# Performance work log

Measured on AMD Instinct MI355X. Metric: run time of the kernel, lower is better.

Reference implementation:

```python
import jax, jax.numpy as jnp
import numpy as np

N = 30000      # input points
M = 7500       # sampled queries = floor(N * ratio), ratio=0.25
K = 16         # neighbors per query
D_X = 64       # input feature dim
D_REL = 64     # point_pos_nn output dim
D_F = D_X + D_REL  # fij_hat dim = 128


def setup_inputs() -> dict:
    key = jax.random.key(0)
    ks = jax.random.split(key, 6)
    x = jax.random.normal(ks[0], (N, D_X), jnp.float32)
    pos = jax.random.normal(ks[1], (N, 3), jnp.float32)
    idx = jax.random.randint(ks[2], (M,), 0, N)
    W_pos = jax.random.normal(ks[3], (10, D_REL), jnp.float32) / jnp.sqrt(10.0)
    b_pos = jnp.zeros((D_REL,), jnp.float32)
    W_att = jax.random.normal(ks[4], (D_F, D_F), jnp.float32) / jnp.sqrt(float(D_F))
    b_att = jnp.zeros((D_F,), jnp.float32)
    W_glob = jax.random.normal(ks[5], (D_F, D_F), jnp.float32) / jnp.sqrt(float(D_F))
    b_glob = jnp.zeros((D_F,), jnp.float32)
    return {"x": x, "pos": pos, "idx": idx, "W_pos": W_pos, "b_pos": b_pos,
            "W_att": W_att, "b_att": b_att, "W_glob": W_glob, "b_glob": b_glob}


def reference(x, pos, idx, W_pos, b_pos, W_att, b_att, W_glob, b_glob):
    # --- KNN: brute-force squared distances from sampled queries to all points ---
    pos_q = pos[idx]                                         # [M, 3]
    d2 = ((pos_q * pos_q).sum(-1)[:, None]
          + (pos * pos).sum(-1)[None, :]
          - 2.0 * pos_q @ pos.T)                             # [M, N]
    _, nbr = jax.lax.top_k(-d2, K)                           # [M, K] neighbor indices

    # --- Local Spatial Encoding (message) ---
    pos_j = pos[nbr]                                         # [M, K, 3]
    pos_i = jnp.broadcast_to(pos_q[:, None, :], pos_j.shape) # [M, K, 3]
    vij = pos_i - pos_j                                      # [M, K, 3]
    dij = jnp.linalg.norm(vij, axis=-1, keepdims=True)       # [M, K, 1]
    rel = jnp.concatenate([pos_i, pos_j, vij, dij], axis=-1) # [M, K, 10]
    rij = jax.nn.relu(rel @ W_pos + b_pos)                   # [M, K, D_REL]

    # --- Attentive pooling ---
    fij = jnp.concatenate([x[nbr], rij], axis=-1)            # [M, K, D_F]
    g = fij @ W_att + b_att                                  # [M, K, D_F]
    s = jax.nn.softmax(g, axis=-1)                           # softmax over feature dim
    aggr = jnp.mean(s * fij, axis=1)                         # mean over K neighbors -> [M, D_F]

    # --- global_nn (update) ---
    return jax.nn.relu(aggr @ W_glob + b_glob)               # [M, D_F]
```

## Files before the change

kernel.cpp:

```cpp
#include <hip/hip_runtime.h>
#include <stdint.h>

#define KNB     16
#define GD      64
#define GTOT    (GD * GD * GD)
#define GORIG   (-6.5f)
#define GEDGE   0.203125f
#define GINV    (1.0f / GEDGE)
#define CAPW    640
#define PROBE_T 48

typedef short short8 __attribute__((ext_vector_type(8)));
typedef float floatx4 __attribute__((ext_vector_type(4)));

__device__ __forceinline__ unsigned short f2bf(float x) {
  union { float f; uint32_t u; } v; v.f = x;
  uint32_t u = v.u + 0x7FFFu + ((v.u >> 16) & 1u);
  return (unsigned short)(u >> 16);
}
__device__ __forceinline__ float bf2f(unsigned short b) {
  return __uint_as_float(((uint32_t)b) << 16);
}
__device__ __forceinline__ int cellco(float v) {
  int c = (int)floorf((v - GORIG) * GINV);
  return c < 0 ? 0 : (c > GD - 1 ? GD - 1 : c);
}

__global__ void zero_kernel(int* __restrict__ count) {
  int i = (blockIdx.x * 256 + threadIdx.x) * 4;
  *(int4*)(count + i) = make_int4(0, 0, 0, 0);
}

__global__ void prep_kernel(const float* __restrict__ x,
                            const float* __restrict__ pos,
                            const float* __restrict__ W_att,
                            unsigned short* __restrict__ xb,
                            float4* __restrict__ pos4,
                            unsigned short* __restrict__ Wt,
                            int* __restrict__ ptcell,
                            int* __restrict__ count, int N) {
  int id = blockIdx.x * 256 + threadIdx.x;
  int nx8 = N * 8;
  if (id < nx8) {
    const float4* src = (const float4*)x + (size_t)id * 2;
    float4 a = src[0], b = src[1];
    short8 v;
    v[0] = (short)f2bf(a.x); v[1] = (short)f2bf(a.y);
    v[2] = (short)f2bf(a.z); v[3] = (short)f2bf(a.w);
    v[4] = (short)f2bf(b.x); v[5] = (short)f2bf(b.y);
    v[6] = (short)f2bf(b.z); v[7] = (short)f2bf(b.w);
    *(short8*)(xb + (size_t)id * 8) = v;
  } else if (id < nx8 + N) {
    int j = id - nx8;
    float px = pos[3 * j], py = pos[3 * j + 1], pz = pos[3 * j + 2];
    float pp = fmaf(px, px, fmaf(py, py, pz * pz));
    pos4[j] = make_float4(px, py, pz, pp);
    int cid = (cellco(pz) * GD + cellco(py)) * GD + cellco(px);
    ptcell[j] = cid;
    atomicAdd(&count[cid], 1);
  } else if (id < nx8 + N + 128 * 128) {
    int t = id - nx8 - N;
    int c = t >> 7, f = t & 127;
    Wt[f * 128 + c] = f2bf(W_att[t]);
  }
}

__global__ __launch_bounds__(256) void scan1(const int* __restrict__ count,
                                             int* __restrict__ partial) {
  int b = blockIdx.x, t = threadIdx.x;
  int v = count[b * 256 + t];
#pragma unroll
  for (int off = 1; off < 64; off <<= 1) v += __shfl_xor(v, off);
  __shared__ int ws_[4];
  if ((t & 63) == 0) ws_[t >> 6] = v;
  __syncthreads();
  if (t == 0) partial[b] = ws_[0] + ws_[1] + ws_[2] + ws_[3];
}

__global__ __launch_bounds__(256) void scan2(int* __restrict__ partial,
                                             int* __restrict__ cell_start) {
  int t = threadIdx.x;
  int v0 = partial[t * 4], v1 = partial[t * 4 + 1];
  int v2 = partial[t * 4 + 2], v3 = partial[t * 4 + 3];
  int s1 = v0 + v1, s2 = s1 + v2, s3 = s2 + v3;
  int x = s3;
  int lane = t & 63, wv = t >> 6;
#pragma unroll
  for (int off = 1; off < 64; off <<= 1) {
    int y = __shfl_up(x, off);
    if (lane >= off) x += y;
  }
  __shared__ int wsum[4];
  if (lane == 63) wsum[wv] = x;
  __syncthreads();
  int base = 0;
  for (int k = 0; k < wv; ++k) base += wsum[k];
  int excl = base + x - s3;
  partial[t * 4]     = excl;
  partial[t * 4 + 1] = excl + v0;
  partial[t * 4 + 2] = excl + s1;
  partial[t * 4 + 3] = excl + s2;
  if (t == 255) cell_start[GTOT] = excl + s3;
}

__global__ __launch_bounds__(256) void scan3(const int* __restrict__ count,
                                             const int* __restrict__ partial,
                                             int* __restrict__ cell_start,
                                             int* __restrict__ cursor) {
  int b = blockIdx.x, t = threadIdx.x;
  int v = count[b * 256 + t];
  int x = v;
  int lane = t & 63, wv = t >> 6;
#pragma unroll
  for (int off = 1; off < 64; off <<= 1) {
    int y = __shfl_up(x, off);
    if (lane >= off) x += y;
  }
  __shared__ int wsum[4];
  if (lane == 63) wsum[wv] = x;
  __syncthreads();
  int base = partial[b];
  for (int k = 0; k < wv; ++k) base += wsum[k];
  int excl = base + x - v;
  cell_start[b * 256 + t] = excl;
  cursor[b * 256 + t] = excl;
}

__global__ void scatter_kernel(const float4* __restrict__ pos4,
                               const int* __restrict__ ptcell,
                               int* __restrict__ cursor,
                               float4* __restrict__ spos4,
                               int* __restrict__ sid, int N) {
  int j = blockIdx.x * 256 + threadIdx.x;
  if (j >= N) return;
  int cid = ptcell[j];
  int slot = atomicAdd(&cursor[cid], 1);
  spos4[slot] = pos4[j];
  sid[slot] = j;
}

__global__ __launch_bounds__(256) void vscan_x(const int* __restrict__ count,
                                               int* __restrict__ V) {
  int row = blockIdx.x * 4 + (threadIdx.x >> 6);
  int ln = threadIdx.x & 63;
  int i = row * GD + ln;
  int v = count[i];
#pragma unroll
  for (int off = 1; off < 64; off <<= 1) {
    int y = __shfl_up(v, off);
    if (ln >= off) v += y;
  }
  V[i] = v;
}

__global__ __launch_bounds__(256) void vscan_y(int* __restrict__ V) {
  int pair = blockIdx.x * 4 + (threadIdx.x >> 6);
  int z = pair >> 6, x = pair & 63;
  int ln = threadIdx.x & 63;
  int i = (z * GD + ln) * GD + x;
  int v = V[i];
#pragma unroll
  for (int off = 1; off < 64; off <<= 1) {
    int y = __shfl_up(v, off);
    if (ln >= off) v += y;
  }
  V[i] = v;
}

__global__ __launch_bounds__(256) void vscan_z(int* __restrict__ V) {
  int pair = blockIdx.x * 4 + (threadIdx.x >> 6);
  int ln = threadIdx.x & 63;
  int i = ln * GD * GD + pair;
  int v = V[i];
#pragma unroll
  for (int off = 1; off < 64; off <<= 1) {
    int y = __shfl_up(v, off);
    if (ln >= off) v += y;
  }
  V[i] = v;
}

__device__ __forceinline__ unsigned long long top16_reg(
    unsigned long long* candw, int tot, int ln) {
  unsigned long long c[CAPW / 64];
#pragma unroll
  for (int chk = 0; chk < CAPW / 64; ++chk) {
    int slot = chk * 64 + ln;
    c[chk] = (slot < tot) ? candw[slot] : ~0ull;
  }
  unsigned long long mykey = ~0ull, last = 0;
#pragma unroll
  for (int r = 0; r < KNB; ++r) {
    unsigned long long mn = c[0];
#pragma unroll
    for (int chk = 1; chk < CAPW / 64; ++chk) mn = (c[chk] < mn) ? c[chk] : mn;
#pragma unroll
    for (int off = 1; off < 64; off <<= 1) {
      unsigned long long o = __shfl_xor(mn, off);
      mn = (o < mn) ? o : mn;
    }
    if (ln == r) mykey = mn;
    last = mn;
#pragma unroll
    for (int chk = 0; chk < CAPW / 64; ++chk)
      if (c[chk] == mn) c[chk] = ~0ull;
  }
  if (ln < KNB) candw[ln] = mykey;
  return last;
}

__device__ __forceinline__ void drain_annulus(
    const float4* __restrict__ spos4, const int* __restrict__ sid,
    const int* __restrict__ cell_start, unsigned long long* candw,
    uint32_t* rsAw, uint32_t* rlAw, uint32_t* rsBw, uint32_t* rpsw,
    float4 qp, int cqx, int cqy, int cqz, int slo, int shi, int ln,
    int& tot, unsigned long long& taukey) {
  const int z0 = (cqz - shi < 0) ? 0 : cqz - shi;
  const int z1 = (cqz + shi > GD - 1) ? GD - 1 : cqz + shi;
  const int y0 = (cqy - shi < 0) ? 0 : cqy - shi;
  const int y1 = (cqy + shi > GD - 1) ? GD - 1 : cqy + shi;
  const int wy = y1 - y0 + 1;
  const int npair = (z1 - z0 + 1) * wy;
  for (int base = 0; base < npair; base += 64) {
    int i = base + ln;
    int stA = 0, lA = 0, stB = 0, lB = 0;
    if (i < npair) {
      int zz = z0 + i / wy;
      int yy = y0 + (i - (i / wy) * wy);
      int dz = zz - cqz, dy = yy - cqy;
      int az = dz < 0 ? -dz : dz, ay = dy < 0 ? -dy : dy;
      int ch = az > ay ? az : ay;
      int rowbase = (zz * GD + yy) * GD;
      if (ch > slo) {
        int x0 = cqx - shi; if (x0 < 0) x0 = 0;
        int x1 = cqx + shi; if (x1 > GD - 1) x1 = GD - 1;
        stA = cell_start[rowbase + x0];
        lA  = cell_start[rowbase + x1 + 1] - stA;
      } else {
        int xl0 = cqx - shi; if (xl0 < 0) xl0 = 0;
        int xl1 = cqx - slo - 1;
        if (xl1 >= xl0) {
          stA = cell_start[rowbase + xl0];
          lA  = cell_start[rowbase + xl1 + 1] - stA;
        }
        int xr0 = cqx + slo + 1;
        int xr1 = cqx + shi; if (xr1 > GD - 1) xr1 = GD - 1;
        if (xr1 >= xr0) {
          stB = cell_start[rowbase + xr0];
          lB  = cell_start[rowbase + xr1 + 1] - stB;
        }
      }
    }
    int len = lA + lB;
    int xinc = len;
#pragma unroll
    for (int off = 1; off < 64; off <<= 1) {
      int y = __shfl_up(xinc, off);
      if (ln >= off) xinc += y;
    }
    int T = __shfl(xinc, 63);
    if (T == 0) continue;
    rpsw[ln] = (uint32_t)(xinc - len);
    rsAw[ln] = (uint32_t)stA;
    rlAw[ln] = (uint32_t)lA;
    rsBw[ln] = (uint32_t)stB;
    for (int b2 = 0; b2 < T; b2 += 64) {
      if (tot + 64 > CAPW) {
        taukey = top16_reg(candw, tot, ln);
        tot = KNB;
      }
      int flat = b2 + ln;
      unsigned long long key = ~0ull;
      bool ok = false;
      if (flat < T) {
        int lo = 0;
#pragma unroll
        for (int step = 32; step > 0; step >>= 1) {
          int mid = lo + step;
          if (mid <= 63 && (int)rpsw[mid] <= flat) lo = mid;
        }
        int o = flat - (int)rpsw[lo];
        uint32_t sa = rsAw[lo], la = rlAw[lo];
        int p = (o < (int)la) ? (int)(sa + o)
                              : (int)(rsBw[lo] + (uint32_t)(o - (int)la));
        float4 pj = spos4[p];
        float dot = fmaf(qp.x, pj.x, fmaf(qp.y, pj.y, qp.z * pj.z));
        float tt  = fmaf(-2.f, dot, pj.w);
        float d2  = fmaxf(qp.w + tt, 0.f);
        key = ((unsigned long long)__float_as_uint(d2) << 32) |
              (uint32_t)sid[p];
        ok = key < taukey;
      }
      unsigned long long bm = __ballot(ok);
      int pos = __popcll(bm & ((1ull << ln) - 1ull));
      if (ok) candw[tot + pos] = key;
      tot += __popcll(bm);
    }
  }
}

__global__ __launch_bounds__(256) void knn_grid(
    const float4* __restrict__ pos4, const float4* __restrict__ spos4,
    const int* __restrict__ sid, const int* __restrict__ cell_start,
    const int* __restrict__ V, const int* __restrict__ idx,
    int* __restrict__ nbr, int M) {
  __shared__ unsigned long long cand[4][CAPW];
  __shared__ uint32_t rsA[4][64], rlA[4][64], rsB[4][64], rps[4][64];
  const int tid = threadIdx.x, wv = tid >> 6, ln = tid & 63;
  const int m = blockIdx.x * 4 + wv;
  if (m >= M) return;

  const float4 qp = pos4[idx[m]];
  const int cqx = cellco(qp.x), cqy = cellco(qp.y), cqz = cellco(qp.z);

  int s0;
  {
    int s = ln;
    int xh = cqx + s > GD - 1 ? GD - 1 : cqx + s;
    int yh = cqy + s > GD - 1 ? GD - 1 : cqy + s;
    int zh = cqz + s > GD - 1 ? GD - 1 : cqz + s;
    int xm = cqx - s - 1, ym = cqy - s - 1, zm = cqz - s - 1;
    int c = V[(zh * GD + yh) * GD + xh];
    if (zm >= 0) c -= V[(zm * GD + yh) * GD + xh];
    if (ym >= 0) c -= V[(zh * GD + ym) * GD + xh];
    if (xm >= 0) c -= V[(zh * GD + yh) * GD + xm];
    if (zm >= 0 && ym >= 0) c += V[(zm * GD + ym) * GD + xh];
    if (zm >= 0 && xm >= 0) c += V[(zm * GD + yh) * GD + xm];
    if (ym >= 0 && xm >= 0) c += V[(zh * GD + ym) * GD + xm];
    if (zm >= 0 && ym >= 0 && xm >= 0) c -= V[(zm * GD + ym) * GD + xm];
    unsigned long long bm = __ballot(c >= PROBE_T);
    s0 = __ffsll((unsigned long long)bm) - 1;
  }

  int tot = 0;
  unsigned long long taukey = ~0ull;
  drain_annulus(spos4, sid, cell_start, &cand[wv][0], &rsA[wv][0],
                &rlA[wv][0], &rsB[wv][0], &rps[wv][0], qp, cqx, cqy, cqz,
                -1, s0, ln, tot, taukey);
  taukey = top16_reg(&cand[wv][0], tot, ln);
  tot = KNB;
  float d16sq = __uint_as_float((uint32_t)(taukey >> 32));

  int s1 = s0;
  {
    float fx = qp.x - GORIG, fy = qp.y - GORIG, fz = qp.z - GORIG;
    while (s1 < GD - 1) {
      float r = 3.0e38f;
      if (cqx - s1 > 0)      r = fminf(r, fx - (float)(cqx - s1) * GEDGE);
      if (cqx + s1 < GD - 1) r = fminf(r, (float)(cqx + s1 + 1) * GEDGE - fx);
      if (cqy - s1 > 0)      r = fminf(r, fy - (float)(cqy - s1) * GEDGE);
      if (cqy + s1 < GD - 1) r = fminf(r, (float)(cqy + s1 + 1) * GEDGE - fy);
      if (cqz - s1 > 0)      r = fminf(r, fz - (float)(cqz - s1) * GEDGE);
      if (cqz + s1 < GD - 1) r = fminf(r, (float)(cqz + s1 + 1) * GEDGE - fz);
      float r2 = (r > 1.0e19f) ? 3.0e38f : r * r;
      if (r2 >= d16sq) break;
      ++s1;
    }
  }

  if (s1 > s0) {
    drain_annulus(spos4, sid, cell_start, &cand[wv][0], &rsA[wv][0],
                  &rlA[wv][0], &rsB[wv][0], &rps[wv][0], qp, cqx, cqy, cqz,
                  s0, s1, ln, tot, taukey);
    if (tot > KNB) (void)top16_reg(&cand[wv][0], tot, ln);
  }

  if (ln < KNB) nbr[m * KNB + ln] = (int)(uint32_t)cand[wv][ln];
}

__global__ __launch_bounds__(256) void mid_kernel(
    const unsigned short* __restrict__ xb, const float4* __restrict__ pos4,
    const int* __restrict__ idx, const float* __restrict__ W_pos,
    const float* __restrict__ b_pos, const unsigned short* __restrict__ Wt,
    const float* __restrict__ b_att, const int* __restrict__ nbr,
    float* __restrict__ aggr, int M) {
  __shared__ __align__(16) unsigned short fijb[8][16][136];
  __shared__ int nbr_s[128];
  __shared__ float4 qpos_s[8];

  const int tid = threadIdx.x;
  const int wid = tid >> 6, lane = tid & 63;
  const int col = lane & 15, quad = lane >> 4;
  const int b = blockIdx.x;

  if (tid < 128) {
    int mq = b * 8 + (tid >> 4); if (mq >= M) mq = M - 1;
    nbr_s[tid] = nbr[mq * 16 + (tid & 15)];
  }
  if (tid < 8) {
    int mq = b * 8 + tid; if (mq >= M) mq = M - 1;
    qpos_s[tid] = pos4[idx[mq]];
  }
  float wp[10];
#pragma unroll
  for (int t = 0; t < 10; ++t) wp[t] = W_pos[t * 64 + lane];
  float bp = b_pos[lane];
  __syncthreads();

  {
    int rr = tid >> 1, h = tid & 1;
    int jn = nbr_s[rr];
    const short8* src = (const short8*)(xb + ((size_t)jn << 6) + (h << 5));
    short8 v0 = src[0], v1 = src[1], v2 = src[2], v3 = src[3];
    short8* dst = (short8*)&fijb[rr >> 4][rr & 15][h * 32];
    dst[0] = v0; dst[1] = v1; dst[2] = v2; dst[3] = v3;
  }
#pragma unroll
  for (int qi = 0; qi < 2; ++qi) {
    int q = wid * 2 + qi;
    float4 qp = qpos_s[q];
#pragma unroll 4
    for (int k = 0; k < 16; ++k) {
      int jn = nbr_s[q * 16 + k];
      float4 pj = pos4[jn];
      float vx = qp.x - pj.x, vy = qp.y - pj.y, vz = qp.z - pj.z;
      float dd = sqrtf(fmaf(vx, vx, fmaf(vy, vy, vz * vz)));
      float r = bp;
      r = fmaf(qp.x, wp[0], r); r = fmaf(qp.y, wp[1], r); r = fmaf(qp.z, wp[2], r);
      r = fmaf(pj.x, wp[3], r); r = fmaf(pj.y, wp[4], r); r = fmaf(pj.z, wp[5], r);
      r = fmaf(vx, wp[6], r);  r = fmaf(vy, wp[7], r);  r = fmaf(vz, wp[8], r);
      r = fmaf(dd, wp[9], r);
      r = fmaxf(r, 0.f);
      fijb[q][k][64 + lane] = f2bf(r);
    }
  }
  __syncthreads();

#pragma unroll 1
  for (int qi = 0; qi < 2; ++qi) {
    int q = wid * 2 + qi;
    int mq = b * 8 + q;

    short8 af[4];
#pragma unroll
    for (int cs = 0; cs < 4; ++cs)
      af[cs] = *(const short8*)&fijb[q][col][cs * 32 + quad * 8];

    floatx4 acc[8];
#pragma unroll
    for (int ft = 0; ft < 8; ++ft) {
      float bav = b_att[ft * 16 + col];
      floatx4 a = {bav, bav, bav, bav};
#pragma unroll
      for (int cs = 0; cs < 4; ++cs) {
        short8 bfrag =
            *(const short8*)&Wt[(ft * 16 + col) * 128 + cs * 32 + quad * 8];
        a = __builtin_amdgcn_mfma_f32_16x16x32_bf16(af[cs], bfrag, a, 0, 0, 0);
      }
      acc[ft] = a;
    }

    float rowmax[4], rowinv[4];
#pragma unroll
    for (int r = 0; r < 4; ++r) {
      float mx = acc[0][r];
#pragma unroll
      for (int ft = 1; ft < 8; ++ft) mx = fmaxf(mx, acc[ft][r]);
      mx = fmaxf(mx, __shfl_xor(mx, 1));
      mx = fmaxf(mx, __shfl_xor(mx, 2));
      mx = fmaxf(mx, __shfl_xor(mx, 4));
      mx = fmaxf(mx, __shfl_xor(mx, 8));
      float sm = 0.f;
#pragma unroll
      for (int ft = 0; ft < 8; ++ft) sm += __expf(acc[ft][r] - mx);
      sm += __shfl_xor(sm, 1);
      sm += __shfl_xor(sm, 2);
      sm += __shfl_xor(sm, 4);
      sm += __shfl_xor(sm, 8);
      rowmax[r] = mx;
      rowinv[r] = 1.0f / sm;
    }

#pragma unroll
    for (int ft = 0; ft < 8; ++ft) {
      float ap = 0.f;
#pragma unroll
      for (int r = 0; r < 4; ++r) {
        float s = __expf(acc[ft][r] - rowmax[r]) * rowinv[r];
        float fv = bf2f(fijb[q][quad * 4 + r][ft * 16 + col]);
        ap = fmaf(s, fv, ap);
      }
      ap += __shfl_xor(ap, 16);
      ap += __shfl_xor(ap, 32);
      if (quad == 0 && mq < M)
        aggr[mq * 128 + ft * 16 + col] = ap * (1.0f / 16.0f);
    }
  }
}

__global__ __launch_bounds__(256) void out_kernel(
    const float* __restrict__ aggr, const float* __restrict__ W_glob,
    const float* __restrict__ b_glob, float* __restrict__ out, int M) {
  __shared__ float ag[16][128];
  const int tid = threadIdx.x;
  const int mbase = blockIdx.x * 16;
  for (int s = tid; s < 16 * 128; s += 256) {
    int r = s >> 7, cc = s & 127;
    int m = mbase + r;
    ((float*)ag)[s] = (m < M) ? aggr[m * 128 + cc] : 0.0f;
  }
  __syncthreads();
  const int f = tid & 127, h = tid >> 7;
  float acc[8];
  float bg = b_glob[f];
#pragma unroll
  for (int i = 0; i < 8; ++i) acc[i] = bg;
  for (int c = 0; c < 128; c += 4) {
    float w0 = W_glob[(c + 0) * 128 + f];
    float w1 = W_glob[(c + 1) * 128 + f];
    float w2 = W_glob[(c + 2) * 128 + f];
    float w3 = W_glob[(c + 3) * 128 + f];
#pragma unroll
    for (int i = 0; i < 8; ++i) {
      const floatx4 a4 = *(const floatx4*)&ag[h * 8 + i][c];
      acc[i] += a4[0] * w0 + a4[1] * w1 + a4[2] * w2 + a4[3] * w3;
    }
  }
#pragma unroll
  for (int i = 0; i < 8; ++i) {
    int m = mbase + h * 8 + i;
    if (m < M) out[m * 128 + f] = fmaxf(acc[i], 0.0f);
  }
}

extern "C" void kernel_launch(void* const* d_in, const int* in_sizes, int n_in,
                              void* d_out, int out_size, void* d_ws,
                              size_t ws_size, hipStream_t stream) {
  const float* x      = (const float*)d_in[0];
  const float* pos    = (const float*)d_in[1];
  const int*   idx    = (const int*)d_in[2];
  const float* W_pos  = (const float*)d_in[3];
  const float* b_pos  = (const float*)d_in[4];
  const float* W_att  = (const float*)d_in[5];
  const float* b_att  = (const float*)d_in[6];
  const float* W_glob = (const float*)d_in[7];
  const float* b_glob = (const float*)d_in[8];
  float* out = (float*)d_out;

  const int N = in_sizes[1] / 3;
  const int M = in_sizes[2];

  char* ws = (char*)d_ws;
  size_t o = 0;
  float4* pos4 = (float4*)(ws + o);               o += ((size_t)N * 16 + 255) & ~(size_t)255;
  unsigned short* xb = (unsigned short*)(ws + o); o += ((size_t)N * 128 + 255) & ~(size_t)255;
  unsigned short* Wt = (unsigned short*)(ws + o); o += (128 * 128 * 2 + 255) & ~(size_t)255;
  int* nbr = (int*)(ws + o);                      o += (((size_t)M * KNB * 4) + 255) & ~(size_t)255;
  int* ptcell = (int*)(ws + o);                   o += (((size_t)N * 4) + 255) & ~(size_t)255;
  int* count = (int*)(ws + o);                    o += ((size_t)GTOT * 4 + 255) & ~(size_t)255;
  int* cursor = (int*)(ws + o);                   o += ((size_t)GTOT * 4 + 255) & ~(size_t)255;
  int* cell_start = (int*)(ws + o);               o += ((size_t)(GTOT + 1) * 4 + 255) & ~(size_t)255;
  int* V = (int*)(ws + o);                        o += ((size_t)GTOT * 4 + 255) & ~(size_t)255;
  int* partial = (int*)(ws + o);                  o += (1024 * 4 + 255) & ~(size_t)255;
  float4* spos4 = (float4*)(ws + o);              o += ((size_t)N * 16 + 255) & ~(size_t)255;
  int* sid = (int*)(ws + o);                      o += (((size_t)N * 4) + 255) & ~(size_t)255;
  float* aggr = (float*)(ws + o);                 o += ((size_t)M * 128 * 4 + 255) & ~(size_t)255;

  zero_kernel<<<GTOT / 1024, 256, 0, stream>>>(count);

  int prep_ids = N * 8 + N + 128 * 128;
  prep_kernel<<<(prep_ids + 255) / 256, 256, 0, stream>>>(
      x, pos, W_att, xb, pos4, Wt, ptcell, count, N);

  scan1<<<GTOT / 256, 256, 0, stream>>>(count, partial);
  scan2<<<1, 256, 0, stream>>>(partial, cell_start);
  scan3<<<GTOT / 256, 256, 0, stream>>>(count, partial, cell_start, cursor);

  scatter_kernel<<<(N + 255) / 256, 256, 0, stream>>>(pos4, ptcell, cursor,
                                                      spos4, sid, N);

  vscan_x<<<1024, 256, 0, stream>>>(count, V);
  vscan_y<<<1024, 256, 0, stream>>>(V);
  vscan_z<<<1024, 256, 0, stream>>>(V);

  knn_grid<<<(M + 3) / 4, 256, 0, stream>>>(pos4, spos4, sid, cell_start, V,
                                            idx, nbr, M);

  mid_kernel<<<(M + 7) / 8, 256, 0, stream>>>(xb, pos4, idx, W_pos, b_pos, Wt,
                                              b_att, nbr, aggr, M);
  out_kernel<<<(M + 15) / 16, 256, 0, stream>>>(aggr, W_glob, b_glob, out, M);
}
```

Before: 208.2 us.

## Derive cell starts from 3D prefix sums and use shuffles in annulus drain

Drops the three-kernel linear scan (scan1/scan2/scan3) and instead computes each cell's start offset by inclusion-exclusion over the existing 3D inclusive prefix-sum volume, in one derive kernel. This saves two launches and the single-block serial stage. In the KNN annulus drain, the per-wave shared-memory staging arrays used for the binary search are replaced by wave shuffles of register values, removing LDS writes and reads. The shuffle search now runs for every lane, with inactive lanes clamped to the last valid index and a duplicate spos4 load, which adds some shuffle work per iteration.

```diff
diff --git a/kernel.cpp b/kernel.cpp
--- a/kernel.cpp
+++ b/kernel.cpp
@@ -65,65 +65,67 @@
   }
 }
 
-__global__ __launch_bounds__(256) void scan1(const int* __restrict__ count,
-                                             int* __restrict__ partial) {
-  int b = blockIdx.x, t = threadIdx.x;
-  int v = count[b * 256 + t];
-#pragma unroll
-  for (int off = 1; off < 64; off <<= 1) v += __shfl_xor(v, off);
-  __shared__ int ws_[4];
-  if ((t & 63) == 0) ws_[t >> 6] = v;
-  __syncthreads();
-  if (t == 0) partial[b] = ws_[0] + ws_[1] + ws_[2] + ws_[3];
-}
-
-__global__ __launch_bounds__(256) void scan2(int* __restrict__ partial,
-                                             int* __restrict__ cell_start) {
-  int t = threadIdx.x;
-  int v0 = partial[t * 4], v1 = partial[t * 4 + 1];
-  int v2 = partial[t * 4 + 2], v3 = partial[t * 4 + 3];
-  int s1 = v0 + v1, s2 = s1 + v2, s3 = s2 + v3;
-  int x = s3;
-  int lane = t & 63, wv = t >> 6;
+__global__ __launch_bounds__(256) void vscan_x(const int* __restrict__ count,
+                                               int* __restrict__ V) {
+  int row = blockIdx.x * 4 + (threadIdx.x >> 6);
+  int ln = threadIdx.x & 63;
+  int i = row * GD + ln;
+  int v = count[i];
 #pragma unroll
   for (int off = 1; off < 64; off <<= 1) {
-    int y = __shfl_up(x, off);
-    if (lane >= off) x += y;
-  }
-  __shared__ int wsum[4];
-  if (lane == 63) wsum[wv] = x;
-  __syncthreads();
-  int base = 0;
-  for (int k = 0; k < wv; ++k) base += wsum[k];
-  int excl = base + x - s3;
-  partial[t * 4]     = excl;
-  partial[t * 4 + 1] = excl + v0;
-  partial[t * 4 + 2] = excl + s1;
-  partial[t * 4 + 3] = excl + s2;
-  if (t == 255) cell_start[GTOT] = excl + s3;
-}
-
-__global__ __launch_bounds__(256) void scan3(const int* __restrict__ count,
-                                             const int* __restrict__ partial,
-                                             int* __restrict__ cell_start,
-                                             int* __restrict__ cursor) {
-  int b = blockIdx.x, t = threadIdx.x;
-  int v = count[b * 256 + t];
-  int x = v;
-  int lane = t & 63, wv = t >> 6;
+    int y = __shfl_up(v, off);
+    if (ln >= off) v += y;
+  }
+  V[i] = v;
+}
+
+__global__ __launch_bounds__(256) void vscan_y(int* __restrict__ V) {
+  int pair = blockIdx.x * 4 + (threadIdx.x >> 6);
+  int z = pair >> 6, x = pair & 63;
+  int ln = threadIdx.x & 63;
+  int i = (z * GD + ln) * GD + x;
+  int v = V[i];
 #pragma unroll
   for (int off = 1; off < 64; off <<= 1) {
-    int y = __shfl_up(x, off);
-    if (lane >= off) x += y;
-  }
-  __shared__ int wsum[4];
-  if (lane == 63) wsum[wv] = x;
-  __syncthreads();
-  int base = partial[b];
-  for (int k = 0; k < wv; ++k) base += wsum[k];
-  int excl = base + x - v;
-  cell_start[b * 256 + t] = excl;
-  cursor[b * 256 + t] = excl;
+    int y = __shfl_up(v, off);
+    if (ln >= off) v += y;
+  }
+  V[i] = v;
+}
+
+__global__ __launch_bounds__(256) void vscan_z(int* __restrict__ V) {
+  int pair = blockIdx.x * 4 + (threadIdx.x >> 6);
+  int ln = threadIdx.x & 63;
+  int i = ln * GD * GD + pair;
+  int v = V[i];
+#pragma unroll
+  for (int off = 1; off < 64; off <<= 1) {
+    int y = __shfl_up(v, off);
+    if (ln >= off) v += y;
+  }
+  V[i] = v;
+}
+
+__global__ __launch_bounds__(256) void derive_kernel(
+    const int* __restrict__ V, int* __restrict__ cell_start,
+    int* __restrict__ cursor) {
+  int cid = blockIdx.x * 256 + threadIdx.x;
+  int x = cid & 63, y = (cid >> 6) & 63, z = cid >> 12;
+  int s = 0;
+  if (z > 0) s += V[((z - 1) * GD + 63) * GD + 63];
+  if (y > 0) {
+    s += V[(z * GD + (y - 1)) * GD + 63];
+    if (z > 0) s -= V[((z - 1) * GD + (y - 1)) * GD + 63];
+  }
+  if (x > 0) {
+    s += V[(z * GD + y) * GD + (x - 1)];
+    if (y > 0) s -= V[(z * GD + (y - 1)) * GD + (x - 1)];
+    if (z > 0) s -= V[((z - 1) * GD + y) * GD + (x - 1)];
+    if (z > 0 && y > 0) s += V[((z - 1) * GD + (y - 1)) * GD + (x - 1)];
+  }
+  cell_start[cid] = s;
+  cursor[cid] = s;
+  if (cid == 0) cell_start[GTOT] = V[GTOT - 1];
 }
 
 __global__ void scatter_kernel(const float4* __restrict__ pos4,
@@ -139,47 +141,6 @@
   sid[slot] = j;
 }
 
-__global__ __launch_bounds__(256) void vscan_x(const int* __restrict__ count,
-                                               int* __restrict__ V) {
-  int row = blockIdx.x * 4 + (threadIdx.x >> 6);
-  int ln = threadIdx.x & 63;
-  int i = row * GD + ln;
-  int v = count[i];
-#pragma unroll
-  for (int off = 1; off < 64; off <<= 1) {
-    int y = __shfl_up(v, off);
-    if (ln >= off) v += y;
-  }
-  V[i] = v;
-}
-
-__global__ __launch_bounds__(256) void vscan_y(int* __restrict__ V) {
-  int pair = blockIdx.x * 4 + (threadIdx.x >> 6);
-  int z = pair >> 6, x = pair & 63;
-  int ln = threadIdx.x & 63;
-  int i = (z * GD + ln) * GD + x;
-  int v = V[i];
-#pragma unroll
-  for (int off = 1; off < 64; off <<= 1) {
-    int y = __shfl_up(v, off);
-    if (ln >= off) v += y;
-  }
-  V[i] = v;
-}
-
-__global__ __launch_bounds__(256) void vscan_z(int* __restrict__ V) {
-  int pair = blockIdx.x * 4 + (threadIdx.x >> 6);
-  int ln = threadIdx.x & 63;
-  int i = ln * GD * GD + pair;
-  int v = V[i];
-#pragma unroll
-  for (int off = 1; off < 64; off <<= 1) {
-    int y = __shfl_up(v, off);
-    if (ln >= off) v += y;
-  }
-  V[i] = v;
-}
-
 __device__ __forceinline__ unsigned long long top16_reg(
     unsigned long long* candw, int tot, int ln) {
   unsigned long long c[CAPW / 64];
@@ -212,7 +173,6 @@
 __device__ __forceinline__ void drain_annulus(
     const float4* __restrict__ spos4, const int* __restrict__ sid,
     const int* __restrict__ cell_start, unsigned long long* candw,
-    uint32_t* rsAw, uint32_t* rlAw, uint32_t* rsBw, uint32_t* rpsw,
     float4 qp, int cqx, int cqy, int cqz, int slo, int shi, int ln,
     int& tot, unsigned long long& taukey) {
   const int z0 = (cqz - shi < 0) ? 0 : cqz - shi;
@@ -260,37 +220,36 @@
     }
     int T = __shfl(xinc, 63);
     if (T == 0) continue;
-    rpsw[ln] = (uint32_t)(xinc - len);
-    rsAw[ln] = (uint32_t)stA;
-    rlAw[ln] = (uint32_t)lA;
-    rsBw[ln] = (uint32_t)stB;
+    int ps_ex = xinc - len;
+
     for (int b2 = 0; b2 < T; b2 += 64) {
       if (tot + 64 > CAPW) {
         taukey = top16_reg(candw, tot, ln);
         tot = KNB;
       }
       int flat = b2 + ln;
-      unsigned long long key = ~0ull;
-      bool ok = false;
-      if (flat < T) {
-        int lo = 0;
-#pragma unroll
-        for (int step = 32; step > 0; step >>= 1) {
-          int mid = lo + step;
-          if (mid <= 63 && (int)rpsw[mid] <= flat) lo = mid;
-        }
-        int o = flat - (int)rpsw[lo];
-        uint32_t sa = rsAw[lo], la = rlAw[lo];
-        int p = (o < (int)la) ? (int)(sa + o)
-                              : (int)(rsBw[lo] + (uint32_t)(o - (int)la));
-        float4 pj = spos4[p];
-        float dot = fmaf(qp.x, pj.x, fmaf(qp.y, pj.y, qp.z * pj.z));
-        float tt  = fmaf(-2.f, dot, pj.w);
-        float d2  = fmaxf(qp.w + tt, 0.f);
-        key = ((unsigned long long)__float_as_uint(d2) << 32) |
-              (uint32_t)sid[p];
-        ok = key < taukey;
+      bool valid = flat < T;
+      int flatc = valid ? flat : (T - 1);
+      int lo = 0;
+#pragma unroll
+      for (int step = 32; step > 0; step >>= 1) {
+        int mid = lo + step;
+        int v = __shfl(ps_ex, mid & 63);
+        if (mid <= 63 && v <= flatc) lo = mid;
       }
+      int psl = __shfl(ps_ex, lo);
+      int sa  = __shfl(stA, lo);
+      int la  = __shfl(lA, lo);
+      int sb  = __shfl(stB, lo);
+      int o = flatc - psl;
+      int p = (o < la) ? (sa + o) : (sb + (o - la));
+      float4 pj = spos4[p];
+      float dot = fmaf(qp.x, pj.x, fmaf(qp.y, pj.y, qp.z * pj.z));
+      float tt  = fmaf(-2.f, dot, pj.w);
+      float d2  = fmaxf(qp.w + tt, 0.f);
+      unsigned long long key =
+          ((unsigned long long)__float_as_uint(d2) << 32) | (uint32_t)sid[p];
+      bool ok = valid && (key < taukey);
       unsigned long long bm = __ballot(ok);
       int pos = __popcll(bm & ((1ull << ln) - 1ull));
       if (ok) candw[tot + pos] = key;
@@ -305,7 +264,6 @@
     const int* __restrict__ V, const int* __restrict__ idx,
     int* __restrict__ nbr, int M) {
   __shared__ unsigned long long cand[4][CAPW];
-  __shared__ uint32_t rsA[4][64], rlA[4][64], rsB[4][64], rps[4][64];
   const int tid = threadIdx.x, wv = tid >> 6, ln = tid & 63;
   const int m = blockIdx.x * 4 + wv;
   if (m >= M) return;
@@ -334,8 +292,7 @@
 
   int tot = 0;
   unsigned long long taukey = ~0ull;
-  drain_annulus(spos4, sid, cell_start, &cand[wv][0], &rsA[wv][0],
-                &rlA[wv][0], &rsB[wv][0], &rps[wv][0], qp, cqx, cqy, cqz,
+  drain_annulus(spos4, sid, cell_start, &cand[wv][0], qp, cqx, cqy, cqz,
                 -1, s0, ln, tot, taukey);
   taukey = top16_reg(&cand[wv][0], tot, ln);
   tot = KNB;
@@ -359,8 +316,7 @@
   }
 
   if (s1 > s0) {
-    drain_annulus(spos4, sid, cell_start, &cand[wv][0], &rsA[wv][0],
-                  &rlA[wv][0], &rsB[wv][0], &rps[wv][0], qp, cqx, cqy, cqz,
+    drain_annulus(spos4, sid, cell_start, &cand[wv][0], qp, cqx, cqy, cqz,
                   s0, s1, ln, tot, taukey);
     if (tot > KNB) (void)top16_reg(&cand[wv][0], tot, ln);
   }
@@ -551,7 +507,6 @@
   int* cursor = (int*)(ws + o);                   o += ((size_t)GTOT * 4 + 255) & ~(size_t)255;
   int* cell_start = (int*)(ws + o);               o += ((size_t)(GTOT + 1) * 4 + 255) & ~(size_t)255;
   int* V = (int*)(ws + o);                        o += ((size_t)GTOT * 4 + 255) & ~(size_t)255;
-  int* partial = (int*)(ws + o);                  o += (1024 * 4 + 255) & ~(size_t)255;
   float4* spos4 = (float4*)(ws + o);              o += ((size_t)N * 16 + 255) & ~(size_t)255;
   int* sid = (int*)(ws + o);                      o += (((size_t)N * 4) + 255) & ~(size_t)255;
   float* aggr = (float*)(ws + o);                 o += ((size_t)M * 128 * 4 + 255) & ~(size_t)255;
@@ -562,16 +517,13 @@
   prep_kernel<<<(prep_ids + 255) / 256, 256, 0, stream>>>(
       x, pos, W_att, xb, pos4, Wt, ptcell, count, N);
 
-  scan1<<<GTOT / 256, 256, 0, stream>>>(count, partial);
-  scan2<<<1, 256, 0, stream>>>(partial, cell_start);
-  scan3<<<GTOT / 256, 256, 0, stream>>>(count, partial, cell_start, cursor);
-
-  scatter_kernel<<<(N + 255) / 256, 256, 0, stream>>>(pos4, ptcell, cursor,
-                                                      spos4, sid, N);
-
   vscan_x<<<1024, 256, 0, stream>>>(count, V);
   vscan_y<<<1024, 256, 0, stream>>>(V);
   vscan_z<<<1024, 256, 0, stream>>>(V);
+  derive_kernel<<<GTOT / 256, 256, 0, stream>>>(V, cell_start, cursor);
+
+  scatter_kernel<<<(N + 255) / 256, 256, 0, stream>>>(pos4, ptcell, cursor,
+                                                      spos4, sid, N);
 
   knn_grid<<<(M + 3) / 4, 256, 0, stream>>>(pos4, spos4, sid, cell_start, V,
                                             idx, nbr, M);
```

Measured after the change: 203.8 us. -2.2%, faster.
